# Performance work log

Measured on AMD Instinct MI355X. Metric: run time of the kernel, lower is better.

## Reference

```python
import jax, jax.numpy as jnp
import numpy as np

B, FIN, H, W = 16, 256, 32, 32
NH, FH = 8, 64
CIN = FIN + 2  # fin + 2 coordinate-grid pos channels
COUT = NH * FH


def setup_inputs() -> dict:
    key = jax.random.key(0)
    ks = jax.random.split(key, 9)
    s = 1.0 / np.sqrt(CIN)
    so = 1.0 / np.sqrt(COUT)
    return {
        "x": jax.random.normal(ks[0], (B, FIN, H, W), dtype=jnp.float32),
        "wq": jax.random.uniform(ks[1], (COUT, CIN), jnp.float32, -s, s),
        "bq": jax.random.uniform(ks[2], (COUT,), jnp.float32, -s, s),
        "wk": jax.random.uniform(ks[3], (COUT, CIN), jnp.float32, -s, s),
        "bk": jax.random.uniform(ks[4], (COUT,), jnp.float32, -s, s),
        "wv": jax.random.uniform(ks[5], (COUT, CIN), jnp.float32, -s, s),
        "bv": jax.random.uniform(ks[6], (COUT,), jnp.float32, -s, s),
        "wo": jax.random.uniform(ks[7], (FIN, COUT), jnp.float32, -so, so),
        "bo": jax.random.uniform(ks[8], (FIN,), jnp.float32, -so, so),
    }


def reference(x, wq, bq, wk, bk, wv, bv, wo, bo):
    b, c, h, w = x.shape
    n = h * w
    # PosEncoding: concat one linspace(-1,1) coordinate channel per spatial dim
    gy, gx = jnp.meshgrid(jnp.linspace(-1.0, 1.0, h), jnp.linspace(-1.0, 1.0, w), indexing="ij")
    pos = jnp.broadcast_to(jnp.stack([gy, gx])[None], (b, 2, h, w)).astype(x.dtype)
    t = jnp.concatenate([x, pos], axis=1).reshape(b, c + 2, n)  # [B, C+2, N]
    # 1x1 convs are per-token GEMMs
    q = (jnp.einsum("oc,bcn->bon", wq, t) + bq[:, None]).reshape(b, NH, FH, n)
    k = (jnp.einsum("oc,bcn->bon", wk, t) + bk[:, None]).reshape(b, NH, FH, n)
    v = (jnp.einsum("oc,bcn->bon", wv, t) + bv[:, None]).reshape(b, NH, FH, n)
    temp = FH ** 0.5
    attn = jax.nn.softmax(jnp.einsum("bhdn,bhdm->bhnm", q, k) / temp, axis=-1)
    o = jnp.einsum("bhnm,bhdm->bhdn", attn, v).reshape(b, NH * FH, n)
    o = jnp.einsum("oc,bcn->bon", wo, o) + bo[:, None]
    return x + o.reshape(b, c, h, w)
```

## Files before the change

### kernel.cpp

```cpp
#include <hip/hip_runtime.h>


typedef unsigned short u16;
typedef unsigned int   u32;
typedef __attribute__((ext_vector_type(8))) short  short8;
typedef __attribute__((ext_vector_type(4))) float  float4_;

#define MFMA16(a, b, c) __builtin_amdgcn_mfma_f32_16x16x32_bf16(a, b, c, 0, 0, 0)

__device__ __forceinline__ float bf2f(u16 u) {
    union { u32 i; float f; } v; v.i = ((u32)u) << 16; return v.f;
}
__device__ __forceinline__ u16 f2bf(float f) {
    union { float f; u32 i; } v; v.f = f;
    u32 r = v.i + 0x7FFFu + ((v.i >> 16) & 1u);
    return (u16)(r >> 16);
}

__global__ __launch_bounds__(256) void prep(
    const float* __restrict__ wq, const float* __restrict__ wk,
    const float* __restrict__ wv, const float* __restrict__ x,
    u16* __restrict__ wb, u16* __restrict__ xT)
{
    __shared__ float Lt[64][65];
    const int bid = blockIdx.x;
    const int tid = threadIdx.x;
    if (bid < 512) {
        int i = bid * 256 + tid;
        int o = i >> 8, c = i & 255;
        size_t si = (size_t)o * 258 + c;
        wb[i]          = f2bf(wq[si]);
        wb[131072 + i] = f2bf(wk[si]);
        wb[262144 + i] = f2bf(wv[si]);
    } else {
        int r = bid - 512;
        int n0 = (r & 15) * 64, c0 = ((r >> 4) & 3) * 64, b = r >> 6;
#pragma unroll
        for (int p = 0; p < 4; ++p) {
            int c = p * 16 + (tid >> 4);
            int nn = (tid & 15) * 4;
            float4 v = *(const float4*)&x[((size_t)(b * 256) + c0 + c) * 1024 + n0 + nn];
            Lt[c][nn + 0] = v.x; Lt[c][nn + 1] = v.y;
            Lt[c][nn + 2] = v.z; Lt[c][nn + 3] = v.w;
        }
        __syncthreads();
#pragma unroll
        for (int p = 0; p < 4; ++p) {
            int n = p * 16 + (tid >> 4);
            int cc = (tid & 15) * 4;
            ushort4 st;
            st.x = f2bf(Lt[cc + 0][n]); st.y = f2bf(Lt[cc + 1][n]);
            st.z = f2bf(Lt[cc + 2][n]); st.w = f2bf(Lt[cc + 3][n]);
            *(ushort4*)&xT[((size_t)(b << 10) + n0 + n) * 256 + c0 + cc] = st;
        }
    }
}

__global__ __launch_bounds__(256) void qkv_mfma(
    const u16* __restrict__ xT, const u16* __restrict__ wb,
    const float* __restrict__ wq, const float* __restrict__ wk,
    const float* __restrict__ wv,
    const float* __restrict__ bq, const float* __restrict__ bk,
    const float* __restrict__ bv,
    u16* __restrict__ qkvbuf)
{
    __shared__ u16 Wl[128][40];
    __shared__ u16 Tl[128][40];
    const int tid = threadIdx.x;
    const int lane = tid & 63, w = tid >> 6;
    const int quad = lane >> 4, m15 = lane & 15;
    const int n0 = blockIdx.x * 128, mt = blockIdx.y, b = blockIdx.z;
    const int mat = mt >> 2;
    const int m0 = mt * 128;
    const float* worig = (mat == 0) ? wq : ((mat == 1) ? wk : wv);
    const float* bias  = (mat == 0) ? bq : ((mat == 1) ? bk : bv);
    const float oscale = (mat == 1) ? 0.125f : 1.0f;
    u16* outbuf = qkvbuf + (size_t)mat * 8388608;

    float4_ acc[2][8];
#pragma unroll
    for (int s = 0; s < 2; ++s)
#pragma unroll
        for (int t = 0; t < 8; ++t) acc[s][t] = (float4_){0, 0, 0, 0};

    const int row = tid >> 2, col8 = (tid & 3) * 8;

    for (int cc0 = 0; cc0 < 256; cc0 += 32) {
        __syncthreads();
#pragma unroll
        for (int rr = 0; rr < 128; rr += 64) {
            *(short8*)&Wl[row + rr][col8] =
                *(const short8*)(wb + (size_t)(m0 + row + rr) * 256 + cc0 + col8);
            *(short8*)&Tl[row + rr][col8] =
                *(const short8*)(xT + ((size_t)(b << 10) + n0 + row + rr) * 256 + cc0 + col8);
        }
        __syncthreads();
        short8 af[2];
#pragma unroll
        for (int s = 0; s < 2; ++s)
            af[s] = *(const short8*)&Wl[w * 32 + s * 16 + m15][quad * 8];
#pragma unroll
        for (int t = 0; t < 8; ++t) {
            short8 bf = *(const short8*)&Tl[t * 16 + m15][quad * 8];
#pragma unroll
            for (int s = 0; s < 2; ++s)
                acc[s][t] = MFMA16(af[s], bf, acc[s][t]);
        }
    }

#pragma unroll
    for (int s = 0; s < 2; ++s) {
        float wg[4], wx[4], bi[4];
#pragma unroll
        for (int r = 0; r < 4; ++r) {
            int om = (mt & 3) * 128 + w * 32 + s * 16 + quad * 4 + r;
            wg[r] = worig[(size_t)om * 258 + 256];
            wx[r] = worig[(size_t)om * 258 + 257];
            bi[r] = bias[om];
        }
        const int h = (mt & 3) * 2 + ((w * 32 + s * 16) >> 6);
        const int dbase = ((w * 32 + s * 16) & 63) + quad * 4;
#pragma unroll
        for (int t = 0; t < 8; ++t) {
            int n = n0 + t * 16 + m15;
            float gy = -1.0f + 2.0f * (float)(n >> 5) / 31.0f;
            float gx = -1.0f + 2.0f * (float)(n & 31) / 31.0f;
            float v[4];
#pragma unroll
            for (int r = 0; r < 4; ++r)
                v[r] = (acc[s][t][r] + wg[r] * gy + wx[r] * gx + bi[r]) * oscale;
            if (mat != 2) {
                ushort4 st;
                st.x = f2bf(v[0]); st.y = f2bf(v[1]);
                st.z = f2bf(v[2]); st.w = f2bf(v[3]);
                *(ushort4*)&outbuf[((size_t)(b * 8 + h) * 1024 + n) * 64 + dbase] = st;
            } else {
#pragma unroll
                for (int r = 0; r < 4; ++r)
                    outbuf[((size_t)(b * 8 + h) * 64 + dbase + r) * 1024 + n] = f2bf(v[r]);
            }
        }
    }
}

__global__ __launch_bounds__(256) void attn_mfma(
    u16* __restrict__ qbuf, const u16* __restrict__ kbuf,
    const u16* __restrict__ vbuf)
{
    __shared__ u16 Kl[64 * 64];
    __shared__ u16 Vl[64 * 64];
    __shared__ u16 Pl[4][2][16][72];

    const int tid = threadIdx.x;
    const int lane = tid & 63, w = tid >> 6;
    const int quad = lane >> 4, m15 = lane & 15;
    const int bh = blockIdx.x;
    const int q0 = blockIdx.y * 128;
    u16* qb = qbuf + (size_t)bh * 65536;
    const u16* kb = kbuf + (size_t)bh * 65536;
    const u16* vb = vbuf + (size_t)bh * 65536;

    short8 qf[2][2];
#pragma unroll
    for (int s = 0; s < 2; ++s) {
        const u16* qr = qb + (size_t)(q0 + w * 32 + s * 16 + m15) * 64 + quad * 8;
        qf[s][0] = *(const short8*)qr;
        qf[s][1] = *(const short8*)(qr + 32);
    }

    float4_ O[2][4];
    float lp[2] = {0.0f, 0.0f};
#pragma unroll
    for (int s = 0; s < 2; ++s)
#pragma unroll
        for (int t = 0; t < 4; ++t) O[s][t] = (float4_){0,0,0,0};

    const int row = tid >> 3, c8 = (tid & 7) * 8;
    const int stsw = c8 ^ ((row & 7) << 3);
    const int rdsw = (m15 & 7) << 3;
    const int psw  = (m15 & 3) << 3;

    for (int kt0 = 0; kt0 < 1024; kt0 += 64) {
        __syncthreads();
#pragma unroll
        for (int rr = 0; rr < 64; rr += 32) {
            *(short8*)&Kl[(row + rr) * 64 + stsw] =
                *(const short8*)(kb + (size_t)(kt0 + row + rr) * 64 + c8);
            *(short8*)&Vl[(row + rr) * 64 + stsw] =
                *(const short8*)(vb + (size_t)(row + rr) * 1024 + kt0 + c8);
        }
        __syncthreads();

        float4_ S[2][4];
#pragma unroll
        for (int s = 0; s < 2; ++s)
#pragma unroll
            for (int t = 0; t < 4; ++t) S[s][t] = (float4_){0, 0, 0, 0};
#pragma unroll
        for (int c = 0; c < 2; ++c) {
            short8 kf[4];
#pragma unroll
            for (int t = 0; t < 4; ++t)
                kf[t] = *(const short8*)&Kl[(t * 16 + m15) * 64 +
                                            ((c * 32 + quad * 8) ^ rdsw)];
            __builtin_amdgcn_s_setprio(1);
#pragma unroll
            for (int s = 0; s < 2; ++s)
#pragma unroll
                for (int t = 0; t < 4; ++t)
                    S[s][t] = MFMA16(kf[t], qf[s][c], S[s][t]);
            __builtin_amdgcn_s_setprio(0);
        }

#pragma unroll
        for (int s = 0; s < 2; ++s) {
            float lsum = 0.0f;
#pragma unroll
            for (int t = 0; t < 4; ++t) {
                float p0 = __expf(S[s][t][0]);
                float p1 = __expf(S[s][t][1]);
                float p2 = __expf(S[s][t][2]);
                float p3 = __expf(S[s][t][3]);
                u32 w0, w1;
                asm("v_cvt_pk_bf16_f32 %0, %1, %2" : "=v"(w0) : "v"(p0), "v"(p1));
                asm("v_cvt_pk_bf16_f32 %0, %1, %2" : "=v"(w1) : "v"(p2), "v"(p3));
                const int col = (t * 16 + quad * 4) ^ psw;
                uint2 st; st.x = w0; st.y = w1;
                *(uint2*)&Pl[w][s][m15][col] = st;
                lsum += (p0 + p1) + (p2 + p3);
            }
            lp[s] += lsum;
        }

#pragma unroll
        for (int c = 0; c < 2; ++c) {
            short8 av[4];
#pragma unroll
            for (int dt = 0; dt < 4; ++dt)
                av[dt] = *(const short8*)&Vl[(dt * 16 + m15) * 64 +
                                             ((c * 32 + quad * 8) ^ rdsw)];
#pragma unroll
            for (int s = 0; s < 2; ++s) {
                short8 bp = *(const short8*)&Pl[w][s][m15][(c * 32 + quad * 8) ^ psw];
                __builtin_amdgcn_s_setprio(1);
#pragma unroll
                for (int dt = 0; dt < 4; ++dt)
                    O[s][dt] = MFMA16(av[dt], bp, O[s][dt]);
                __builtin_amdgcn_s_setprio(0);
            }
        }
    }

#pragma unroll
    for (int s = 0; s < 2; ++s) {
        float v = lp[s];
        v += __shfl_xor(v, 16);
        v += __shfl_xor(v, 32);
        float linv = 1.0f / v;
        int n = q0 + w * 32 + s * 16 + m15;
#pragma unroll
        for (int dt = 0; dt < 4; ++dt) {
            ushort4 st;
            st.x = f2bf(O[s][dt][0] * linv);
            st.y = f2bf(O[s][dt][1] * linv);
            st.z = f2bf(O[s][dt][2] * linv);
            st.w = f2bf(O[s][dt][3] * linv);
            *(ushort4*)&qb[(size_t)n * 64 + dt * 16 + quad * 4] = st;
        }
    }
}

__global__ __launch_bounds__(256) void proj_mfma(
    const u16* __restrict__ ao, const float* __restrict__ wo,
    const float* __restrict__ bo, const float* __restrict__ x,
    float* __restrict__ out)
{
    __shared__ u16 Wl[64][72];
    __shared__ u16 Tl[64][72];
    const int tid = threadIdx.x;
    const int lane = tid & 63, w = tid >> 6;
    const int quad = lane >> 4, m15 = lane & 15;
    const int n0 = blockIdx.x * 64, f0 = blockIdx.y * 64, b = blockIdx.z;

    float4_ acc[4] = {{0,0,0,0},{0,0,0,0},{0,0,0,0},{0,0,0,0}};
    const int row = tid >> 3, c8 = (tid & 7) * 8;

    for (int cc0 = 0; cc0 < 512; cc0 += 64) {
        __syncthreads();
        const int h = cc0 >> 6;
#pragma unroll
        for (int rr = 0; rr < 64; rr += 32) {
            const float* wsrc = wo + (size_t)(f0 + row + rr) * 512 + cc0 + c8;
            float4 v0 = *(const float4*)wsrc;
            float4 v1 = *(const float4*)(wsrc + 4);
            ushort4 s0, s1;
            s0.x = f2bf(v0.x); s0.y = f2bf(v0.y); s0.z = f2bf(v0.z); s0.w = f2bf(v0.w);
            s1.x = f2bf(v1.x); s1.y = f2bf(v1.y); s1.z = f2bf(v1.z); s1.w = f2bf(v1.w);
            *(ushort4*)&Wl[row + rr][c8]     = s0;
            *(ushort4*)&Wl[row + rr][c8 + 4] = s1;
            *(short8*)&Tl[row + rr][c8] =
                *(const short8*)(ao + ((size_t)((b << 3) + h) * 1024 + n0 + row + rr) * 64 + c8);
        }
        __syncthreads();
#pragma unroll
        for (int c = 0; c < 2; ++c) {
            short8 af = *(const short8*)&Wl[w * 16 + m15][c * 32 + quad * 8];
#pragma unroll
            for (int t = 0; t < 4; ++t) {
                short8 bf = *(const short8*)&Tl[t * 16 + m15][c * 32 + quad * 8];
                acc[t] = MFMA16(af, bf, acc[t]);
            }
        }
    }

    float bi[4];
#pragma unroll
    for (int r = 0; r < 4; ++r) bi[r] = bo[f0 + w * 16 + quad * 4 + r];
#pragma unroll
    for (int t = 0; t < 4; ++t) {
        int n = n0 + t * 16 + m15;
#pragma unroll
        for (int r = 0; r < 4; ++r) {
            int f = f0 + w * 16 + quad * 4 + r;
            size_t idx = ((size_t)(b * 256) + f) * 1024 + n;
            out[idx] = acc[t][r] + bi[r] + x[idx];
        }
    }
}

extern "C" void kernel_launch(void* const* d_in, const int* in_sizes, int n_in,
                              void* d_out, int out_size, void* d_ws, size_t ws_size,
                              hipStream_t stream) {
    const float* x  = (const float*)d_in[0];
    const float* wq = (const float*)d_in[1];
    const float* bq = (const float*)d_in[2];
    const float* wk = (const float*)d_in[3];
    const float* bk = (const float*)d_in[4];
    const float* wv = (const float*)d_in[5];
    const float* bv = (const float*)d_in[6];
    const float* wo = (const float*)d_in[7];
    const float* bo = (const float*)d_in[8];

    u16* qkvbuf = (u16*)d_ws;
    u16* region = qkvbuf + 3 * 8388608;
    u16* xT = region;
    u16* wb = region + 4194304;

    prep<<<1536, 256, 0, stream>>>(wq, wk, wv, x, wb, xT);

    qkv_mfma<<<dim3(8, 12, 16), 256, 0, stream>>>(
        xT, wb, wq, wk, wv, bq, bk, bv, qkvbuf);

    attn_mfma<<<dim3(128, 8), 256, 0, stream>>>(
        qkvbuf, qkvbuf + 8388608, qkvbuf + 16777216);

    proj_mfma<<<dim3(16, 4, 16), 256, 0, stream>>>(qkvbuf, wo, bo, x, (float*)d_out);
}
```

Before: 199.3 us.

## Halve attention query tile per block, use exp2 with folded log2e scale

The attention kernel now handles 64 queries per block (16 per wave) instead of 128, doubling the grid to 2048 blocks. The aim is better occupancy and load balance at the cost of loading each K/V tile twice as often. The K scale now folds in log2(e), so the softmax can use the raw v_exp_f32 instruction instead of __expf. The P staging layout in shared memory is also rearranged into 8-element chunks with no swizzle, which may change LDS bank conflicts.

```diff
diff --git a/kernel.cpp b/kernel.cpp
--- a/kernel.cpp
+++ b/kernel.cpp
@@ -15,6 +15,11 @@
     union { float f; u32 i; } v; v.f = f;
     u32 r = v.i + 0x7FFFu + ((v.i >> 16) & 1u);
     return (u16)(r >> 16);
+}
+__device__ __forceinline__ float exp2_fast(float x) {
+    float r;
+    asm("v_exp_f32 %0, %1" : "=v"(r) : "v"(x));
+    return r;
 }
 
 __global__ __launch_bounds__(256) void prep(
@@ -74,7 +79,7 @@
     const int m0 = mt * 128;
     const float* worig = (mat == 0) ? wq : ((mat == 1) ? wk : wv);
     const float* bias  = (mat == 0) ? bq : ((mat == 1) ? bk : bv);
-    const float oscale = (mat == 1) ? 0.125f : 1.0f;
+    const float oscale = (mat == 1) ? 0.1803368801111204f : 1.0f;
     u16* outbuf = qkvbuf + (size_t)mat * 8388608;
 
     float4_ acc[2][8];
@@ -149,36 +154,32 @@
 {
     __shared__ u16 Kl[64 * 64];
     __shared__ u16 Vl[64 * 64];
-    __shared__ u16 Pl[4][2][16][72];
+    __shared__ u16 Pl[4][8][16][8];
 
     const int tid = threadIdx.x;
     const int lane = tid & 63, w = tid >> 6;
     const int quad = lane >> 4, m15 = lane & 15;
     const int bh = blockIdx.x;
-    const int q0 = blockIdx.y * 128;
+    const int q0 = blockIdx.y * 64;
     u16* qb = qbuf + (size_t)bh * 65536;
     const u16* kb = kbuf + (size_t)bh * 65536;
     const u16* vb = vbuf + (size_t)bh * 65536;
 
-    short8 qf[2][2];
-#pragma unroll
-    for (int s = 0; s < 2; ++s) {
-        const u16* qr = qb + (size_t)(q0 + w * 32 + s * 16 + m15) * 64 + quad * 8;
-        qf[s][0] = *(const short8*)qr;
-        qf[s][1] = *(const short8*)(qr + 32);
-    }
-
-    float4_ O[2][4];
-    float lp[2] = {0.0f, 0.0f};
-#pragma unroll
-    for (int s = 0; s < 2; ++s)
-#pragma unroll
-        for (int t = 0; t < 4; ++t) O[s][t] = (float4_){0,0,0,0};
+    short8 qf[2];
+    {
+        const u16* qr = qb + (size_t)(q0 + w * 16 + m15) * 64 + quad * 8;
+        qf[0] = *(const short8*)qr;
+        qf[1] = *(const short8*)(qr + 32);
+    }
+
+    float4_ O[4];
+    float lp = 0.0f;
+#pragma unroll
+    for (int t = 0; t < 4; ++t) O[t] = (float4_){0, 0, 0, 0};
 
     const int row = tid >> 3, c8 = (tid & 7) * 8;
     const int stsw = c8 ^ ((row & 7) << 3);
     const int rdsw = (m15 & 7) << 3;
-    const int psw  = (m15 & 3) << 3;
 
     for (int kt0 = 0; kt0 < 1024; kt0 += 64) {
         __syncthreads();
@@ -191,11 +192,9 @@
         }
         __syncthreads();
 
-        float4_ S[2][4];
-#pragma unroll
-        for (int s = 0; s < 2; ++s)
-#pragma unroll
-            for (int t = 0; t < 4; ++t) S[s][t] = (float4_){0, 0, 0, 0};
+        float4_ S[4];
+#pragma unroll
+        for (int t = 0; t < 4; ++t) S[t] = (float4_){0, 0, 0, 0};
 #pragma unroll
         for (int c = 0; c < 2; ++c) {
             short8 kf[4];
@@ -205,31 +204,27 @@
                                             ((c * 32 + quad * 8) ^ rdsw)];
             __builtin_amdgcn_s_setprio(1);
 #pragma unroll
-            for (int s = 0; s < 2; ++s)
-#pragma unroll
-                for (int t = 0; t < 4; ++t)
-                    S[s][t] = MFMA16(kf[t], qf[s][c], S[s][t]);
+            for (int t = 0; t < 4; ++t)
+                S[t] = MFMA16(kf[t], qf[c], S[t]);
             __builtin_amdgcn_s_setprio(0);
         }
 
-#pragma unroll
-        for (int s = 0; s < 2; ++s) {
+        {
             float lsum = 0.0f;
 #pragma unroll
             for (int t = 0; t < 4; ++t) {
-                float p0 = __expf(S[s][t][0]);
-                float p1 = __expf(S[s][t][1]);
-                float p2 = __expf(S[s][t][2]);
-                float p3 = __expf(S[s][t][3]);
+                float p0 = exp2_fast(S[t][0]);
+                float p1 = exp2_fast(S[t][1]);
+                float p2 = exp2_fast(S[t][2]);
+                float p3 = exp2_fast(S[t][3]);
                 u32 w0, w1;
                 asm("v_cvt_pk_bf16_f32 %0, %1, %2" : "=v"(w0) : "v"(p0), "v"(p1));
                 asm("v_cvt_pk_bf16_f32 %0, %1, %2" : "=v"(w1) : "v"(p2), "v"(p3));
-                const int col = (t * 16 + quad * 4) ^ psw;
                 uint2 st; st.x = w0; st.y = w1;
-                *(uint2*)&Pl[w][s][m15][col] = st;
+                *(uint2*)&Pl[w][t * 2 + (quad >> 1)][m15][(quad & 1) * 4] = st;
                 lsum += (p0 + p1) + (p2 + p3);
             }
-            lp[s] += lsum;
+            lp += lsum;
         }
 
 #pragma unroll
@@ -239,32 +234,28 @@
             for (int dt = 0; dt < 4; ++dt)
                 av[dt] = *(const short8*)&Vl[(dt * 16 + m15) * 64 +
                                              ((c * 32 + quad * 8) ^ rdsw)];
-#pragma unroll
-            for (int s = 0; s < 2; ++s) {
-                short8 bp = *(const short8*)&Pl[w][s][m15][(c * 32 + quad * 8) ^ psw];
-                __builtin_amdgcn_s_setprio(1);
-#pragma unroll
-                for (int dt = 0; dt < 4; ++dt)
-                    O[s][dt] = MFMA16(av[dt], bp, O[s][dt]);
-                __builtin_amdgcn_s_setprio(0);
-            }
-        }
-    }
-
-#pragma unroll
-    for (int s = 0; s < 2; ++s) {
-        float v = lp[s];
+            short8 bp = *(const short8*)&Pl[w][c * 4 + quad][m15][0];
+            __builtin_amdgcn_s_setprio(1);
+#pragma unroll
+            for (int dt = 0; dt < 4; ++dt)
+                O[dt] = MFMA16(av[dt], bp, O[dt]);
+            __builtin_amdgcn_s_setprio(0);
+        }
+    }
+
+    {
+        float v = lp;
         v += __shfl_xor(v, 16);
         v += __shfl_xor(v, 32);
         float linv = 1.0f / v;
-        int n = q0 + w * 32 + s * 16 + m15;
+        int n = q0 + w * 16 + m15;
 #pragma unroll
         for (int dt = 0; dt < 4; ++dt) {
             ushort4 st;
-            st.x = f2bf(O[s][dt][0] * linv);
-            st.y = f2bf(O[s][dt][1] * linv);
-            st.z = f2bf(O[s][dt][2] * linv);
-            st.w = f2bf(O[s][dt][3] * linv);
+            st.x = f2bf(O[dt][0] * linv);
+            st.y = f2bf(O[dt][1] * linv);
+            st.z = f2bf(O[dt][2] * linv);
+            st.w = f2bf(O[dt][3] * linv);
             *(ushort4*)&qb[(size_t)n * 64 + dt * 16 + quad * 4] = st;
         }
     }
@@ -351,7 +342,7 @@
     qkv_mfma<<<dim3(8, 12, 16), 256, 0, stream>>>(
         xT, wb, wq, wk, wv, bq, bk, bv, qkvbuf);
 
-    attn_mfma<<<dim3(128, 8), 256, 0, stream>>>(
+    attn_mfma<<<dim3(128, 16), 256, 0, stream>>>(
         qkvbuf, qkvbuf + 8388608, qkvbuf + 16777216);
 
     proj_mfma<<<dim3(16, 4, 16), 256, 0, stream>>>(qkvbuf, wo, bo, x, (float*)d_out);
```

Result: no change. 200.2 us (+0.4%).
